# Performance work log

Hardware: AMD Instinct MI355X
Metric: run time of the kernel (lower is better)

Reference implementation:

```python
import jax, jax.numpy as jnp
import numpy as np

N_HEAD = 16
HEAD_DIM = 64  # n_embd // n_head = 1024 // 16


def setup_inputs() -> dict:
    key = jax.random.key(0)
    k1, k2, k3 = jax.random.split(key, 3)
    B, T, C = 4, 2048, 1024
    x = jax.random.normal(k1, (B, T, C), dtype=jnp.float32)
    # torch Linear weight is (out, in); we store transposed (in, out) for x @ W
    w_qkv = jax.random.normal(k2, (C, 3 * C), dtype=jnp.float32) * (1.0 / np.sqrt(C))
    w_out = jax.random.normal(k3, (C, C), dtype=jnp.float32) * (1.0 / np.sqrt(C))
    return {"x": x, "w_qkv": w_qkv, "w_out": w_out}


def reference(x, w_qkv, w_out):
    B, T, C = x.shape
    scale = 1.0 / np.sqrt(HEAD_DIM).astype(np.float32)
    qkv = x @ w_qkv                                   # [B, T, 3C]
    q, k, v = jnp.split(qkv, 3, axis=2)
    def heads(t):  # [B, T, C] -> [B, H, T, Dh]
        return t.reshape(B, T, N_HEAD, HEAD_DIM).transpose(0, 2, 1, 3)
    q, k, v = heads(q), heads(k), heads(v)
    att = jnp.einsum('bhqd,bhkd->bhqk', q, k) * scale  # [B, H, T, T]
    causal = jnp.tril(jnp.ones((T, T), dtype=bool))
    att = jnp.where(causal[None, None], att, jnp.float32(-jnp.inf))
    att = jax.nn.softmax(att, axis=-1)
    y = jnp.einsum('bhqk,bhkd->bhqd', att, v)          # [B, H, T, Dh]
    y = y.transpose(0, 2, 1, 3).reshape(B, T, C)
    return y @ w_out
```

## Files before the change

kernel.cpp:

```cpp
#include <hip/hip_runtime.h>
#include <hip/hip_bf16.h>

#define B_ 4
#define T_ 2048
#define C_ 1024
#define H_ 16
#define D_ 64

typedef __bf16 bf16x8 __attribute__((ext_vector_type(8)));
typedef float f32x4 __attribute__((ext_vector_type(4)));
typedef float f32x16 __attribute__((ext_vector_type(16)));

__device__ __forceinline__ unsigned short f2bs(float f) {
    __hip_bfloat16 h = __float2bfloat16(f);
    return *reinterpret_cast<unsigned short*>(&h);
}

__device__ __forceinline__ unsigned cvtpk(float a, float b) {
    unsigned r;
    asm("v_cvt_pk_bf16_f32 %0, %1, %2" : "=v"(r) : "v"(a), "v"(b));
    return r;
}

__device__ __forceinline__ void plane32swap(unsigned& a, unsigned& b, int hi) {
#if __has_builtin(__builtin_amdgcn_permlane32_swap)
    typedef int i32x2 __attribute__((ext_vector_type(2)));
    i32x2 r = __builtin_amdgcn_permlane32_swap((int)a, (int)b, false, false);
    a = (unsigned)r.x; b = (unsigned)r.y;
#else
    unsigned v = hi ? a : b;
    unsigned e = __shfl_xor(v, 32);
    unsigned na = hi ? e : a;
    unsigned nb = hi ? b : e;
    a = na; b = nb;
#endif
}

__device__ __forceinline__ int swz(int row, int col) {
    return (row * 64 + col) ^ ((row & 7) << 3);
}

__device__ __forceinline__ void gload16(const void* g, void* l) {
    auto gp = (const __attribute__((address_space(1))) void*)(g);
    auto lp = (__attribute__((address_space(3))) void*)(uintptr_t)(l);
    __builtin_amdgcn_global_load_lds(gp, lp, 16, 0, 0);
}

__global__ __launch_bounds__(256)
void cvt_f32_to_bf16(const float* __restrict__ in, unsigned short* __restrict__ out, int n4) {
    int i = blockIdx.x * 256 + threadIdx.x;
    if (i >= n4) return;
    float4 v = ((const float4*)in)[i];
    union { unsigned short h[4]; uint2 u; } pk;
    pk.h[0] = f2bs(v.x); pk.h[1] = f2bs(v.y);
    pk.h[2] = f2bs(v.z); pk.h[3] = f2bs(v.w);
    ((uint2*)out)[i] = pk.u;
}

__global__ __launch_bounds__(256)
void transpose_weights(const float* __restrict__ in1, unsigned short* __restrict__ out1,
                       const float* __restrict__ in2, unsigned short* __restrict__ out2) {
    __shared__ float tile[64][65];
    const int tx = threadIdx.x & 63;
    const int ty = threadIdx.x >> 6;
    const bool second = blockIdx.x >= 48;
    const float* in = second ? in2 : in1;
    unsigned short* out = second ? out2 : out1;
    const int C = second ? 1024 : 3072;
    const int R = 1024;
    const int c0 = (second ? (blockIdx.x - 48) : blockIdx.x) * 64;
    const int r0 = blockIdx.y * 64;
    #pragma unroll
    for (int i = 0; i < 16; ++i) {
        int r = ty * 16 + i;
        tile[r][tx] = in[(size_t)(r0 + r) * C + c0 + tx];
    }
    __syncthreads();
    #pragma unroll
    for (int i = 0; i < 16; ++i) {
        int r = ty * 16 + i;
        out[(size_t)(c0 + r) * R + r0 + tx] = f2bs(tile[tx][r]);
    }
}

template<int MODE>
__global__ __launch_bounds__(256)
void gemm_bt(const unsigned short* __restrict__ A,
             const unsigned short* __restrict__ Bt,
             float* __restrict__ Out, int N_out,
             unsigned short* __restrict__ Qb,
             unsigned short* __restrict__ Kb,
             unsigned short* __restrict__ Vt,
             int K) {
    __shared__ alignas(16) unsigned short As[2][128 * 64];
    __shared__ alignas(16) unsigned short Bs[2][128 * 64];
    const int tid = threadIdx.x;
    const int l = tid & 63;
    const int c16 = l & 15, lq = l >> 4;
    const int wv = tid >> 6;
    const int wrow = wv >> 1, wcol = wv & 1;
    const int m0 = blockIdx.x * 128, n0 = blockIdx.y * 128;

    f32x4 acc[4][4];
    #pragma unroll
    for (int i = 0; i < 4; ++i)
        #pragma unroll
        for (int j = 0; j < 4; ++j)
            acc[i][j] = f32x4{0.f, 0.f, 0.f, 0.f};

    const int srow = tid >> 3;
    const int scs  = tid & 7;
    const int ldsbase = (tid & ~63) * 8;

    auto stage = [&](int k0, int buf) {
        #pragma unroll
        for (int p = 0; p < 4; ++p) {
            int row = p * 32 + srow;
            int csw = 8 * (scs ^ (row & 7));
            gload16(&A[(size_t)(m0 + row) * K + k0 + csw], &As[buf][p * 2048 + ldsbase]);
            gload16(&Bt[(size_t)(n0 + row) * K + k0 + csw], &Bs[buf][p * 2048 + ldsbase]);
        }
    };

    stage(0, 0);
    const int NK = K >> 6;
    for (int i = 0; i < NK; ++i) {
        __syncthreads();
        if (i + 1 < NK) stage((i + 1) << 6, (i + 1) & 1);
        const unsigned short* Al = As[i & 1];
        const unsigned short* Bl = Bs[i & 1];
        #pragma unroll
        for (int kk = 0; kk < 64; kk += 32) {
            bf16x8 af[4], bfv[4];
            int koff = kk + lq * 8;
            #pragma unroll
            for (int t = 0; t < 4; ++t) {
                af[t]  = *(const bf16x8*)&Al[swz(wrow * 64 + t * 16 + c16, koff)];
                bfv[t] = *(const bf16x8*)&Bl[swz(wcol * 64 + t * 16 + c16, koff)];
            }
            #pragma unroll
            for (int mi = 0; mi < 4; ++mi)
                #pragma unroll
                for (int ni = 0; ni < 4; ++ni)
                    acc[mi][ni] = __builtin_amdgcn_mfma_f32_16x16x32_bf16(
                        af[mi], bfv[ni], acc[mi][ni], 0, 0, 0);
        }
    }

    #pragma unroll
    for (int mi = 0; mi < 4; ++mi) {
        #pragma unroll
        for (int ni = 0; ni < 4; ++ni) {
            #pragma unroll
            for (int r = 0; r < 4; ++r) {
                float v = acc[mi][ni][r];
                int row = m0 + wrow * 64 + mi * 16 + lq * 4 + r;
                int col = n0 + wcol * 64 + ni * 16 + c16;
                if (MODE == 1) {
                    Out[(size_t)row * N_out + col] = v;
                } else {
                    int which = col >> 10;
                    int c = col & 1023;
                    int h = c >> 6, d = c & 63;
                    int b = row >> 11, t = row & 2047;
                    int bh = b * H_ + h;
                    if (which == 0)
                        Qb[((size_t)(bh * T_ + t)) * D_ + d] = f2bs(v * 0.1803368801111204f);
                    else if (which == 1)
                        Kb[((size_t)(bh * T_ + t)) * D_ + d] = f2bs(v);
                    else
                        Vt[((size_t)(bh * D_ + d)) * T_ + t] = f2bs(v);
                }
            }
        }
    }
}

__global__ __launch_bounds__(256, 4)
void attn_fwd(const unsigned short* __restrict__ Qb,
              const unsigned short* __restrict__ Kb,
              const unsigned short* __restrict__ Vt,
              unsigned short* __restrict__ Y) {
    __shared__ alignas(16) unsigned short Ks[2][64 * 64];
    __shared__ alignas(16) unsigned short Vs[2][64 * 64];
    const int tid = threadIdx.x;
    const int wv = tid >> 6;
    const int l = tid & 63;
    const int r32 = l & 31;
    const int hi = l >> 5;
    const int hi8 = hi * 8;
    const int bh = blockIdx.x & 63;
    const int qc = blockIdx.x >> 6;
    const unsigned short* Kp = Kb + (size_t)bh * T_ * D_;
    const unsigned short* Vp = Vt + (size_t)bh * D_ * T_;
    const unsigned short* Qbase = Qb + (size_t)bh * T_ * D_;
    const int b = bh >> 4, h = bh & 15;
    const int srow = tid >> 3;
    const int scs  = tid & 7;
    const int scol_sw = 8 * (scs ^ (srow & 7));
    const int wbase = wv * 512;

    const int q0w = qc * 128 + wv * 32;
    const int nt = 2 * qc + 2;
    const int qg = q0w + r32;

    bf16x8 qf[4];
    #pragma unroll
    for (int ds = 0; ds < 4; ++ds)
        qf[ds] = *(const bf16x8*)&Qbase[(size_t)qg * 64 + ds * 16 + hi8];

    f32x16 o[2];
    #pragma unroll
    for (int e = 0; e < 16; ++e) { o[0][e] = 0.f; o[1][e] = 0.f; }
    float lsum = 0.f;

    gload16(&Kp[(size_t)srow * 64 + scol_sw],        &Ks[0][wbase]);
    gload16(&Kp[(size_t)(srow + 32) * 64 + scol_sw], &Ks[0][2048 + wbase]);
    gload16(&Vp[(size_t)srow * T_ + scol_sw],        &Vs[0][wbase]);
    gload16(&Vp[(size_t)(srow + 32) * T_ + scol_sw], &Vs[0][2048 + wbase]);

    for (int it = 0; it < nt; ++it) {
        const int kb = it * 64;
        __syncthreads();
        if (it + 1 < nt) {
            const int kn = kb + 64;
            unsigned short* Kd = Ks[(it + 1) & 1];
            unsigned short* Vd = Vs[(it + 1) & 1];
            gload16(&Kp[(size_t)(kn + srow) * 64 + scol_sw],        &Kd[wbase]);
            gload16(&Kp[(size_t)(kn + srow + 32) * 64 + scol_sw],   &Kd[2048 + wbase]);
            gload16(&Vp[(size_t)srow * T_ + kn + scol_sw],          &Vd[wbase]);
            gload16(&Vp[(size_t)(srow + 32) * T_ + kn + scol_sw],   &Vd[2048 + wbase]);
        }
        if (kb > q0w + 31) continue;
        const unsigned short* Kl = Ks[it & 1];
        const unsigned short* Vl = Vs[it & 1];

        f32x16 s[2];
        #pragma unroll
        for (int e = 0; e < 16; ++e) { s[0][e] = 0.f; s[1][e] = 0.f; }
        __builtin_amdgcn_s_setprio(1);
        #pragma unroll
        for (int kt = 0; kt < 2; ++kt)
            #pragma unroll
            for (int ds = 0; ds < 4; ++ds) {
                bf16x8 af = *(const bf16x8*)&Kl[swz(32 * kt + r32, ds * 16 + hi8)];
                s[kt] = __builtin_amdgcn_mfma_f32_32x32x16_bf16(af, qf[ds], s[kt], 0, 0, 0);
            }
        __builtin_amdgcn_s_setprio(0);
        if (kb + 63 > q0w) {
            #pragma unroll
            for (int kt = 0; kt < 2; ++kt)
                #pragma unroll
                for (int m = 0; m < 4; ++m)
                    #pragma unroll
                    for (int r = 0; r < 4; ++r)
                        if (kb + 32 * kt + 8 * m + r + 4 * hi > qg)
                            s[kt][4 * m + r] = -1e30f;
        }
        float rs = 0.f;
        #pragma unroll
        for (int kt = 0; kt < 2; ++kt)
            #pragma unroll
            for (int e = 0; e < 16; ++e) {
                float p = exp2f(s[kt][e]);
                s[kt][e] = p;
                rs += p;
            }
        lsum += rs;
        bf16x8 pb[4];
        #pragma unroll
        for (int ks = 0; ks < 4; ++ks) {
            const int kt = ks >> 1;
            const int m0 = (ks & 1) * 2;
            unsigned a0 = cvtpk(s[kt][4 * m0 + 0], s[kt][4 * m0 + 1]);
            unsigned a1 = cvtpk(s[kt][4 * m0 + 2], s[kt][4 * m0 + 3]);
            unsigned b0 = cvtpk(s[kt][4 * m0 + 4], s[kt][4 * m0 + 5]);
            unsigned b1 = cvtpk(s[kt][4 * m0 + 6], s[kt][4 * m0 + 7]);
            plane32swap(a0, b0, hi);
            plane32swap(a1, b1, hi);
            uint4 u = {a0, a1, b0, b1};
            pb[ks] = *reinterpret_cast<bf16x8*>(&u);
        }
        __builtin_amdgcn_s_setprio(1);
        #pragma unroll
        for (int dt = 0; dt < 2; ++dt)
            #pragma unroll
            for (int ks = 0; ks < 4; ++ks) {
                bf16x8 va = *(const bf16x8*)&Vl[swz(32 * dt + r32, ks * 16 + hi8)];
                o[dt] = __builtin_amdgcn_mfma_f32_32x32x16_bf16(va, pb[ks], o[dt], 0, 0, 0);
            }
        __builtin_amdgcn_s_setprio(0);
    }

    float lt = lsum + __shfl_xor(lsum, 32);
    float inv = 1.f / lt;
    #pragma unroll
    for (int dt = 0; dt < 2; ++dt)
        #pragma unroll
        for (int m = 0; m < 4; ++m) {
            uint2 w;
            w.x = cvtpk(o[dt][4 * m + 0] * inv, o[dt][4 * m + 1] * inv);
            w.y = cvtpk(o[dt][4 * m + 2] * inv, o[dt][4 * m + 3] * inv);
            int d = 32 * dt + 8 * m + 4 * hi;
            *(uint2*)&Y[((size_t)(b * T_ + qg)) * C_ + h * D_ + d] = w;
        }
}

extern "C" void kernel_launch(void* const* d_in, const int* in_sizes, int n_in,
                              void* d_out, int out_size, void* d_ws, size_t ws_size,
                              hipStream_t stream) {
    const float* x     = (const float*)d_in[0];
    const float* w_qkv = (const float*)d_in[1];
    const float* w_out = (const float*)d_in[2];
    float* out = (float*)d_out;
    char* ws = (char*)d_ws;

    unsigned short* xb  = (unsigned short*)(ws);
    unsigned short* wqt = (unsigned short*)(ws + (16u << 20));
    unsigned short* wot = (unsigned short*)(ws + (22u << 20));
    unsigned short* Qb  = (unsigned short*)(ws + (24u << 20));
    unsigned short* Kb  = (unsigned short*)(ws + (40u << 20));
    unsigned short* Vt  = (unsigned short*)(ws + (56u << 20));
    unsigned short* Yb  = (unsigned short*)(ws + (72u << 20));

    cvt_f32_to_bf16<<<8192, 256, 0, stream>>>(x, xb, (B_ * T_ * C_) / 4);
    transpose_weights<<<dim3(64, 16), 256, 0, stream>>>(w_qkv, wqt, w_out, wot);
    gemm_bt<0><<<dim3(64, 24), 256, 0, stream>>>(xb, wqt, nullptr, 3072, Qb, Kb, Vt, 1024);
    attn_fwd<<<1024, 256, 0, stream>>>(Qb, Kb, Vt, Yb);
    gemm_bt<1><<<dim3(64, 8), 256, 0, stream>>>(Yb, wot, out, 1024, nullptr, nullptr, nullptr, 1024);
}
```

Baseline: 177.0 us.

## Load K/V fragments directly from global memory, drop LDS staging and barriers

The attention kernel stops staging K and V tiles in double-buffered shared memory with block-wide barriers. Each wave now loads its MFMA operand fragments straight from global memory, relying on L2/L1 for reuse across waves. Each wave also gets its own causal trip count, and query chunks are launched in reverse order so the heaviest blocks start first. The launch-bounds occupancy hint is dropped. This removes LDS traffic and synchronisation but multiplies global/L2 reads, since four waves reload the same K/V, and increases register pressure.

New measurement: 232.3 us. 1.31x slower.

```diff
diff --git a/kernel.cpp b/kernel.cpp
--- a/kernel.cpp
+++ b/kernel.cpp
@@ -176,13 +176,11 @@
     }
 }
 
-__global__ __launch_bounds__(256, 4)
+__global__ __launch_bounds__(256)
 void attn_fwd(const unsigned short* __restrict__ Qb,
               const unsigned short* __restrict__ Kb,
               const unsigned short* __restrict__ Vt,
               unsigned short* __restrict__ Y) {
-    __shared__ alignas(16) unsigned short Ks[2][64 * 64];
-    __shared__ alignas(16) unsigned short Vs[2][64 * 64];
     const int tid = threadIdx.x;
     const int wv = tid >> 6;
     const int l = tid & 63;
@@ -190,19 +188,15 @@
     const int hi = l >> 5;
     const int hi8 = hi * 8;
     const int bh = blockIdx.x & 63;
-    const int qc = blockIdx.x >> 6;
+    const int qc = 15 - (blockIdx.x >> 6);
     const unsigned short* Kp = Kb + (size_t)bh * T_ * D_;
     const unsigned short* Vp = Vt + (size_t)bh * D_ * T_;
     const unsigned short* Qbase = Qb + (size_t)bh * T_ * D_;
     const int b = bh >> 4, h = bh & 15;
-    const int srow = tid >> 3;
-    const int scs  = tid & 7;
-    const int scol_sw = 8 * (scs ^ (srow & 7));
-    const int wbase = wv * 512;
 
     const int q0w = qc * 128 + wv * 32;
-    const int nt = 2 * qc + 2;
     const int qg = q0w + r32;
+    const int ntw = (q0w + 95) >> 6;
 
     bf16x8 qf[4];
     #pragma unroll
@@ -214,26 +208,16 @@
     for (int e = 0; e < 16; ++e) { o[0][e] = 0.f; o[1][e] = 0.f; }
     float lsum = 0.f;
 
-    gload16(&Kp[(size_t)srow * 64 + scol_sw],        &Ks[0][wbase]);
-    gload16(&Kp[(size_t)(srow + 32) * 64 + scol_sw], &Ks[0][2048 + wbase]);
-    gload16(&Vp[(size_t)srow * T_ + scol_sw],        &Vs[0][wbase]);
-    gload16(&Vp[(size_t)(srow + 32) * T_ + scol_sw], &Vs[0][2048 + wbase]);
-
-    for (int it = 0; it < nt; ++it) {
+    for (int it = 0; it < ntw; ++it) {
         const int kb = it * 64;
-        __syncthreads();
-        if (it + 1 < nt) {
-            const int kn = kb + 64;
-            unsigned short* Kd = Ks[(it + 1) & 1];
-            unsigned short* Vd = Vs[(it + 1) & 1];
-            gload16(&Kp[(size_t)(kn + srow) * 64 + scol_sw],        &Kd[wbase]);
-            gload16(&Kp[(size_t)(kn + srow + 32) * 64 + scol_sw],   &Kd[2048 + wbase]);
-            gload16(&Vp[(size_t)srow * T_ + kn + scol_sw],          &Vd[wbase]);
-            gload16(&Vp[(size_t)(srow + 32) * T_ + kn + scol_sw],   &Vd[2048 + wbase]);
-        }
-        if (kb > q0w + 31) continue;
-        const unsigned short* Kl = Ks[it & 1];
-        const unsigned short* Vl = Vs[it & 1];
+        const unsigned short* Kg = Kp + (size_t)kb * D_;
+
+        bf16x8 kf[2][4];
+        #pragma unroll
+        for (int kt = 0; kt < 2; ++kt)
+            #pragma unroll
+            for (int ds = 0; ds < 4; ++ds)
+                kf[kt][ds] = *(const bf16x8*)&Kg[(32 * kt + r32) * D_ + ds * 16 + hi8];
 
         f32x16 s[2];
         #pragma unroll
@@ -242,11 +226,17 @@
         #pragma unroll
         for (int kt = 0; kt < 2; ++kt)
             #pragma unroll
-            for (int ds = 0; ds < 4; ++ds) {
-                bf16x8 af = *(const bf16x8*)&Kl[swz(32 * kt + r32, ds * 16 + hi8)];
-                s[kt] = __builtin_amdgcn_mfma_f32_32x32x16_bf16(af, qf[ds], s[kt], 0, 0, 0);
-            }
+            for (int ds = 0; ds < 4; ++ds)
+                s[kt] = __builtin_amdgcn_mfma_f32_32x32x16_bf16(kf[kt][ds], qf[ds], s[kt], 0, 0, 0);
         __builtin_amdgcn_s_setprio(0);
+
+        bf16x8 va[2][4];
+        #pragma unroll
+        for (int dt = 0; dt < 2; ++dt)
+            #pragma unroll
+            for (int ks = 0; ks < 4; ++ks)
+                va[dt][ks] = *(const bf16x8*)&Vp[(size_t)(32 * dt + r32) * T_ + kb + ks * 16 + hi8];
+
         if (kb + 63 > q0w) {
             #pragma unroll
             for (int kt = 0; kt < 2; ++kt)
@@ -285,10 +275,8 @@
         #pragma unroll
         for (int dt = 0; dt < 2; ++dt)
             #pragma unroll
-            for (int ks = 0; ks < 4; ++ks) {
-                bf16x8 va = *(const bf16x8*)&Vl[swz(32 * dt + r32, ks * 16 + hi8)];
-                o[dt] = __builtin_amdgcn_mfma_f32_32x32x16_bf16(va, pb[ks], o[dt], 0, 0, 0);
-            }
+            for (int ks = 0; ks < 4; ++ks)
+                o[dt] = __builtin_amdgcn_mfma_f32_32x32x16_bf16(va[dt][ks], pb[ks], o[dt], 0, 0, 0);
         __builtin_amdgcn_s_setprio(0);
     }
 
```
